# Kernel tuning notes

Measured on AMD Instinct MI355X. Metric: run time of the kernel, lower is better.

## Reference

```python
import jax, jax.numpy as jnp
import numpy as np

N_NODES = 100000
N_EDGES = 1600000
HIDDEN = 512
LOWER = 128
NUM_RELS = 6


def setup_inputs() -> dict:
    key = jax.random.key(0)
    ks = jax.random.split(key, 16)
    glorot = lambda k, shape: jax.random.normal(k, shape, jnp.float32) * (2.0 / (shape[-2] + shape[-1])) ** 0.5
    return {
        "h_origin": jax.random.normal(ks[0], (N_NODES, HIDDEN), jnp.float32),
        "edge_src": jax.random.randint(ks[1], (N_EDGES,), 0, N_NODES, jnp.int32),
        "edge_dst": jax.random.randint(ks[2], (N_EDGES,), 0, N_NODES, jnp.int32),
        "edge_type": jax.random.randint(ks[3], (N_EDGES,), 0, NUM_RELS, jnp.int32),
        "W_lower": glorot(ks[4], (HIDDEN, LOWER)),
        "b_lower": jnp.zeros((LOWER,), jnp.float32),
        "W1": glorot(ks[5], (NUM_RELS, LOWER, LOWER)),
        "b1": jnp.zeros((LOWER,), jnp.float32),
        "W2": glorot(ks[6], (NUM_RELS, LOWER, LOWER)),
        "b2": jnp.zeros((LOWER,), jnp.float32),
        "W3": glorot(ks[7], (NUM_RELS, LOWER, LOWER)),
        "b3": jnp.zeros((LOWER,), jnp.float32),
        "W_upper": glorot(ks[8], (LOWER, HIDDEN)),
        "b_upper": jnp.zeros((HIDDEN,), jnp.float32),
        "W_skip": glorot(ks[9], (HIDDEN, HIDDEN)),
        "b_skip": jnp.zeros((HIDDEN,), jnp.float32),
    }


def _ngcn_layer(h, W, b, edge_src, edge_dst, edge_type, n_nodes):
    # R-GCN layer: msg_e = h[src_e] @ W[rel_e]; h'_v = relu(sum_{e->v} msg_e + b)
    # Equivalent grouped form: transform all nodes by all relations (dense GEMMs),
    # then gather per-edge by (rel, src) -- same math as per-edge bmm.
    t = jnp.einsum("nd,rde->rne", h, W)          # [R, N, out]
    msg = t[edge_type, edge_src]                   # [E, out] gather
    agg = jax.ops.segment_sum(msg, edge_dst, num_segments=n_nodes)  # [N, out]
    return jax.nn.relu(agg + b)


def reference(h_origin, edge_src, edge_dst, edge_type,
              W_lower, b_lower, W1, b1, W2, b2, W3, b3,
              W_upper, b_upper, W_skip, b_skip):
    n_nodes = h_origin.shape[0]
    # lower: Linear + ReLU (hidden -> lower)
    h = jax.nn.relu(h_origin @ W_lower + b_lower)
    # three NGCN (R-GCN) layers, num_rels = 6
    h = _ngcn_layer(h, W1, b1, edge_src, edge_dst, edge_type, n_nodes)
    h = _ngcn_layer(h, W2, b2, edge_src, edge_dst, edge_type, n_nodes)
    h = _ngcn_layer(h, W3, b3, edge_src, edge_dst, edge_type, n_nodes)
    # upper(h) + skipper(origin): bg.ndata['h'] = upper(h) + skipper(origin_ndata)
    out = jax.nn.relu(h @ W_upper + b_upper) + jax.nn.relu(h_origin @ W_skip + b_skip)
    return out
```

## Files before the change

### kernel.cpp

```cpp
#include <hip/hip_runtime.h>
#include <hip/hip_bf16.h>

#define NN 100000
#define NE 1600000
#define HID 512
#define LOW 128
#define NR  6
#define NBINS (NN * NR)

typedef short  bf16x8 __attribute__((ext_vector_type(8)));
typedef float  f32x4  __attribute__((ext_vector_type(4)));

__device__ __forceinline__ unsigned short f2bf(float x) {
    __hip_bfloat16 h = __float2bfloat16(x);
    return __builtin_bit_cast(unsigned short, h);
}
__device__ __forceinline__ float bf2f(unsigned short u) {
    return __builtin_bit_cast(float, (unsigned int)u << 16);
}

__device__ __forceinline__ void stage_tile(const unsigned short* __restrict__ G,
                                           int r0, int k0, int Kstride, int Rmax,
                                           char* lds_base, int tid)
{
    #pragma unroll
    for (int is = 0; is < 4; ++is) {
        int L   = is * 4096 + tid * 16;
        int row = L >> 7;
        int c   = ((L >> 4) & 7) ^ (row & 7);
        int gr  = r0 + row;
        gr = (gr < Rmax) ? gr : (Rmax - 1);
        const char* src = (const char*)G + ((size_t)gr * Kstride + k0) * 2 + c * 16;
        __builtin_amdgcn_global_load_lds(
            (const __attribute__((address_space(1))) void*)src,
            (__attribute__((address_space(3))) void*)(lds_base + is * 4096 + (tid & 192) * 16),
            16, 0, 0);
    }
}

__device__ __forceinline__ bf16x8 lds_frag(const char* lds_base, int row, int clog)
{
    return *(const bf16x8*)(lds_base + row * 128 + ((clog ^ (row & 7)) << 4));
}

__global__ __launch_bounds__(256, 2)
void gemm_bf16(const unsigned short* __restrict__ A,
               const unsigned short* __restrict__ Bt,
               const float* __restrict__ bias,
               unsigned short* __restrict__ C,
               int M, int N, int K)
{
    __shared__ __align__(16) char lA[16384];
    __shared__ __align__(16) char lB[16384];

    const int tid  = threadIdx.x;
    const int lane = tid & 63;
    const int wid  = tid >> 6;
    const int wm   = wid >> 1;
    const int wn   = wid & 1;
    const int m0   = blockIdx.y * 128;
    const int n0   = blockIdx.x * 128;

    f32x4 acc[4][4] = {};

    for (int k0 = 0; k0 < K; k0 += 64) {
        stage_tile(A,  m0, k0, K, M, lA, tid);
        stage_tile(Bt, n0, k0, K, N, lB, tid);
        __syncthreads();
        #pragma unroll
        for (int kk = 0; kk < 2; ++kk) {
            const int clog = kk * 4 + (lane >> 4);
            bf16x8 af[4], bfr[4];
            #pragma unroll
            for (int i = 0; i < 4; ++i)
                af[i] = lds_frag(lA, wm * 64 + i * 16 + (lane & 15), clog);
            #pragma unroll
            for (int j = 0; j < 4; ++j)
                bfr[j] = lds_frag(lB, wn * 64 + j * 16 + (lane & 15), clog);
            #pragma unroll
            for (int i = 0; i < 4; ++i)
                #pragma unroll
                for (int j = 0; j < 4; ++j)
                    acc[i][j] = __builtin_amdgcn_mfma_f32_16x16x32_bf16(
                        af[i], bfr[j], acc[i][j], 0, 0, 0);
        }
        __syncthreads();
    }

    const int col_l = lane & 15;
    const int rgrp  = lane >> 4;
    #pragma unroll
    for (int i = 0; i < 4; ++i) {
        #pragma unroll
        for (int j = 0; j < 4; ++j) {
            int col  = n0 + wn * 64 + j * 16 + col_l;
            float bv = bias[col];
            #pragma unroll
            for (int r = 0; r < 4; ++r) {
                int row = m0 + wm * 64 + i * 16 + rgrp * 4 + r;
                if (row < M)
                    C[(size_t)row * N + col] = f2bf(fmaxf(acc[i][j][r] + bv, 0.f));
            }
        }
    }
}

__global__ __launch_bounds__(256, 2)
void gemm_out_fused(const unsigned short* __restrict__ h,
                    const unsigned short* __restrict__ Wut,
                    const float* __restrict__ bu,
                    const unsigned short* __restrict__ hob,
                    const unsigned short* __restrict__ Wst,
                    const float* __restrict__ bs,
                    float* __restrict__ out, int M)
{
    __shared__ __align__(16) char lA[16384];
    __shared__ __align__(16) char lB[16384];

    const int tid  = threadIdx.x;
    const int lane = tid & 63;
    const int wid  = tid >> 6;
    const int wm   = wid >> 1;
    const int wn   = wid & 1;
    const int m0   = blockIdx.y * 128;
    const int n0   = blockIdx.x * 128;

    f32x4 acc1[4][4] = {};
    f32x4 acc2[4][4] = {};

    for (int k0 = 0; k0 < LOW; k0 += 64) {
        stage_tile(h,   m0, k0, LOW, M,   lA, tid);
        stage_tile(Wut, n0, k0, LOW, HID, lB, tid);
        __syncthreads();
        #pragma unroll
        for (int kk = 0; kk < 2; ++kk) {
            const int clog = kk * 4 + (lane >> 4);
            bf16x8 af[4], bfr[4];
            #pragma unroll
            for (int i = 0; i < 4; ++i)
                af[i] = lds_frag(lA, wm * 64 + i * 16 + (lane & 15), clog);
            #pragma unroll
            for (int j = 0; j < 4; ++j)
                bfr[j] = lds_frag(lB, wn * 64 + j * 16 + (lane & 15), clog);
            #pragma unroll
            for (int i = 0; i < 4; ++i)
                #pragma unroll
                for (int j = 0; j < 4; ++j)
                    acc1[i][j] = __builtin_amdgcn_mfma_f32_16x16x32_bf16(
                        af[i], bfr[j], acc1[i][j], 0, 0, 0);
        }
        __syncthreads();
    }
    for (int k0 = 0; k0 < HID; k0 += 64) {
        stage_tile(hob, m0, k0, HID, M,   lA, tid);
        stage_tile(Wst, n0, k0, HID, HID, lB, tid);
        __syncthreads();
        #pragma unroll
        for (int kk = 0; kk < 2; ++kk) {
            const int clog = kk * 4 + (lane >> 4);
            bf16x8 af[4], bfr[4];
            #pragma unroll
            for (int i = 0; i < 4; ++i)
                af[i] = lds_frag(lA, wm * 64 + i * 16 + (lane & 15), clog);
            #pragma unroll
            for (int j = 0; j < 4; ++j)
                bfr[j] = lds_frag(lB, wn * 64 + j * 16 + (lane & 15), clog);
            #pragma unroll
            for (int i = 0; i < 4; ++i)
                #pragma unroll
                for (int j = 0; j < 4; ++j)
                    acc2[i][j] = __builtin_amdgcn_mfma_f32_16x16x32_bf16(
                        af[i], bfr[j], acc2[i][j], 0, 0, 0);
        }
        __syncthreads();
    }

    const int col_l = lane & 15;
    const int rgrp  = lane >> 4;
    #pragma unroll
    for (int i = 0; i < 4; ++i) {
        #pragma unroll
        for (int j = 0; j < 4; ++j) {
            int col   = n0 + wn * 64 + j * 16 + col_l;
            float bv1 = bu[col], bv2 = bs[col];
            #pragma unroll
            for (int r = 0; r < 4; ++r) {
                int row = m0 + wm * 64 + i * 16 + rgrp * 4 + r;
                if (row < M)
                    out[(size_t)row * HID + col] =
                        fmaxf(acc1[i][j][r] + bv1, 0.f) + fmaxf(acc2[i][j][r] + bv2, 0.f);
            }
        }
    }
}

__global__ __launch_bounds__(256)
void conv_f32_bf16(const float4* __restrict__ in, ushort4* __restrict__ out, int n4)
{
    for (int i = blockIdx.x * 256 + threadIdx.x; i < n4; i += gridDim.x * 256) {
        float4 v = in[i];
        ushort4 o;
        o.x = f2bf(v.x); o.y = f2bf(v.y); o.z = f2bf(v.z); o.w = f2bf(v.w);
        out[i] = o;
    }
}

__global__ __launch_bounds__(256)
void transpose_bf16(const float* __restrict__ W, unsigned short* __restrict__ Wt,
                    int R, int C)
{
    int idx = blockIdx.x * 256 + threadIdx.x;
    if (idx < R * C) {
        int r = idx / C, c = idx - r * C;
        Wt[(size_t)c * R + r] = f2bf(W[idx]);
    }
}

#define SCAN_VT 8
#define SCAN_BS 256
#define SCAN_CHUNK (SCAN_VT * SCAN_BS)
#define SCAN_NB ((NBINS + SCAN_CHUNK - 1) / SCAN_CHUNK)

__global__ __launch_bounds__(256)
void k_hist(const int* __restrict__ dst, const int* __restrict__ typ,
            int* __restrict__ deg, int E)
{
    int e = blockIdx.x * 256 + threadIdx.x;
    if (e < E) atomicAdd(&deg[dst[e] * NR + typ[e]], 1);
}

__global__ __launch_bounds__(SCAN_BS)
void k_scan_part(const int* __restrict__ deg, int* __restrict__ blocksum, int n)
{
    __shared__ int ps[SCAN_BS];
    const int t = threadIdx.x;
    const int lo = blockIdx.x * SCAN_CHUNK + t * SCAN_VT;
    int s = 0;
    #pragma unroll
    for (int k = 0; k < SCAN_VT; ++k) {
        int i = lo + k;
        if (i < n) s += deg[i];
    }
    ps[t] = s;
    __syncthreads();
    for (int off = SCAN_BS / 2; off > 0; off >>= 1) {
        if (t < off) ps[t] += ps[t + off];
        __syncthreads();
    }
    if (t == 0) blocksum[blockIdx.x] = ps[0];
}

__global__ __launch_bounds__(64)
void k_scan_mid(const int* __restrict__ blocksum, int* __restrict__ blockoff,
                int* __restrict__ rowstart, int nb, int n)
{
    if (threadIdx.x == 0) {
        int run = 0;
        for (int i = 0; i < nb; ++i) { blockoff[i] = run; run += blocksum[i]; }
        rowstart[n] = run;
    }
}

__global__ __launch_bounds__(SCAN_BS)
void k_scan_final(const int* __restrict__ deg, const int* __restrict__ blockoff,
                  int* __restrict__ rowstart, int* __restrict__ cursor, int n)
{
    __shared__ int ps[SCAN_BS];
    const int t = threadIdx.x;
    const int lo = blockIdx.x * SCAN_CHUNK + t * SCAN_VT;
    int local[SCAN_VT];
    int s = 0;
    #pragma unroll
    for (int k = 0; k < SCAN_VT; ++k) {
        int i = lo + k;
        int v = (i < n) ? deg[i] : 0;
        local[k] = v;
        s += v;
    }
    ps[t] = s;
    __syncthreads();
    for (int off = 1; off < SCAN_BS; off <<= 1) {
        int v = (t >= off) ? ps[t - off] : 0;
        __syncthreads();
        ps[t] += v;
        __syncthreads();
    }
    int run = blockoff[blockIdx.x] + ((t > 0) ? ps[t - 1] : 0);
    #pragma unroll
    for (int k = 0; k < SCAN_VT; ++k) {
        int i = lo + k;
        if (i < n) {
            rowstart[i] = run;
            cursor[i]   = run;
            run += local[k];
        }
    }
}

__global__ __launch_bounds__(256)
void k_fill(const int* __restrict__ src, const int* __restrict__ dst,
            const int* __restrict__ typ, int* __restrict__ cursor,
            int* __restrict__ list, int E)
{
    int e = blockIdx.x * 256 + threadIdx.x;
    if (e < E) {
        int pos = atomicAdd(&cursor[dst[e] * NR + typ[e]], 1);
        list[pos] = src[e];
    }
}

__global__ __launch_bounds__(256)
void gather_agg(const unsigned short* __restrict__ h,
                const int* __restrict__ rowstart,
                const int* __restrict__ list,
                unsigned short* __restrict__ S)
{
    const int v = (blockIdx.x * 256 + threadIdx.x) >> 6;
    if (v >= NN) return;
    const int lane = threadIdx.x & 63;
    const ushort2* hp = (const ushort2*)h;

    const int b0 = rowstart[v * NR + 0];
    const int b1 = rowstart[v * NR + 1];
    const int b2 = rowstart[v * NR + 2];
    const int b3 = rowstart[v * NR + 3];
    const int b4 = rowstart[v * NR + 4];
    const int b5 = rowstart[v * NR + 5];
    const int b6 = rowstart[v * NR + 6];
    const int n0 = b1 - b0, n1 = b2 - b1, n2 = b3 - b2;
    const int n3 = b4 - b3, n4 = b5 - b4, n5 = b6 - b5;
    const int kmax = max(max(max(n0, n1), max(n2, n3)), max(n4, n5));

    float ax0 = 0.f, ay0 = 0.f, ax1 = 0.f, ay1 = 0.f, ax2 = 0.f, ay2 = 0.f;
    float ax3 = 0.f, ay3 = 0.f, ax4 = 0.f, ay4 = 0.f, ax5 = 0.f, ay5 = 0.f;

    for (int k = 0; k < kmax; ++k) {
        int i0 = (k < n0) ? (b0 + k) : 0;
        int i1 = (k < n1) ? (b1 + k) : 0;
        int i2 = (k < n2) ? (b2 + k) : 0;
        int i3 = (k < n3) ? (b3 + k) : 0;
        int i4 = (k < n4) ? (b4 + k) : 0;
        int i5 = (k < n5) ? (b5 + k) : 0;
        int s0 = list[i0], s1 = list[i1], s2 = list[i2];
        int s3 = list[i3], s4 = list[i4], s5 = list[i5];
        ushort2 u0 = hp[(size_t)s0 * 64 + lane];
        ushort2 u1 = hp[(size_t)s1 * 64 + lane];
        ushort2 u2 = hp[(size_t)s2 * 64 + lane];
        ushort2 u3 = hp[(size_t)s3 * 64 + lane];
        ushort2 u4 = hp[(size_t)s4 * 64 + lane];
        ushort2 u5 = hp[(size_t)s5 * 64 + lane];
        ax0 += (k < n0) ? bf2f(u0.x) : 0.f;  ay0 += (k < n0) ? bf2f(u0.y) : 0.f;
        ax1 += (k < n1) ? bf2f(u1.x) : 0.f;  ay1 += (k < n1) ? bf2f(u1.y) : 0.f;
        ax2 += (k < n2) ? bf2f(u2.x) : 0.f;  ay2 += (k < n2) ? bf2f(u2.y) : 0.f;
        ax3 += (k < n3) ? bf2f(u3.x) : 0.f;  ay3 += (k < n3) ? bf2f(u3.y) : 0.f;
        ax4 += (k < n4) ? bf2f(u4.x) : 0.f;  ay4 += (k < n4) ? bf2f(u4.y) : 0.f;
        ax5 += (k < n5) ? bf2f(u5.x) : 0.f;  ay5 += (k < n5) ? bf2f(u5.y) : 0.f;
    }

    ushort2* o = (ushort2*)(S + (size_t)v * (NR * LOW));
    ushort2 w;
    w.x = f2bf(ax0); w.y = f2bf(ay0); o[0 * 64 + lane] = w;
    w.x = f2bf(ax1); w.y = f2bf(ay1); o[1 * 64 + lane] = w;
    w.x = f2bf(ax2); w.y = f2bf(ay2); o[2 * 64 + lane] = w;
    w.x = f2bf(ax3); w.y = f2bf(ay3); o[3 * 64 + lane] = w;
    w.x = f2bf(ax4); w.y = f2bf(ay4); o[4 * 64 + lane] = w;
    w.x = f2bf(ax5); w.y = f2bf(ay5); o[5 * 64 + lane] = w;
}

extern "C" void kernel_launch(void* const* d_in, const int* in_sizes, int n_in,
                              void* d_out, int out_size, void* d_ws, size_t ws_size,
                              hipStream_t stream)
{
    (void)in_sizes; (void)n_in; (void)out_size; (void)ws_size;

    const float* h_origin = (const float*)d_in[0];
    const int*   esrc     = (const int*)d_in[1];
    const int*   edst     = (const int*)d_in[2];
    const int*   etyp     = (const int*)d_in[3];
    const float* W_lower  = (const float*)d_in[4];
    const float* b_lower  = (const float*)d_in[5];
    const float* Wl[3]    = {(const float*)d_in[6], (const float*)d_in[8], (const float*)d_in[10]};
    const float* bl[3]    = {(const float*)d_in[7], (const float*)d_in[9], (const float*)d_in[11]};
    const float* W_upper  = (const float*)d_in[12];
    const float* b_upper  = (const float*)d_in[13];
    const float* W_skip   = (const float*)d_in[14];
    const float* b_skip   = (const float*)d_in[15];
    float*       out      = (float*)d_out;

    unsigned short* hob = (unsigned short*)d_ws;
    unsigned short* h   = hob + (size_t)NN * HID;
    unsigned short* S   = h + (size_t)NN * LOW;
    unsigned short* wlt = S + (size_t)NN * NR * LOW;
    unsigned short* w1t = wlt + (size_t)LOW * HID;
    unsigned short* w2t = w1t + (size_t)LOW * NR * LOW;
    unsigned short* w3t = w2t + (size_t)LOW * NR * LOW;
    unsigned short* wut = w3t + (size_t)LOW * NR * LOW;
    unsigned short* wst = wut + (size_t)HID * LOW;
    int* deg      = (int*)(wst + (size_t)HID * HID);
    int* rowstart = deg + NBINS;
    int* cursor   = rowstart + NBINS + 1;
    int* list     = cursor + NBINS;
    int* blocksum = list + NE;
    int* blockoff = blocksum + SCAN_NB;
    unsigned short* wtL[3] = {w1t, w2t, w3t};

    const unsigned eBlocks = (unsigned)((NE + 255) / 256);
    const unsigned mBlocks = (unsigned)((NN + 127) / 128);

    conv_f32_bf16<<<dim3(2048), dim3(256), 0, stream>>>(
        (const float4*)h_origin, (ushort4*)hob, NN * HID / 4);
    transpose_bf16<<<dim3((HID * LOW + 255) / 256), dim3(256), 0, stream>>>(
        W_lower, wlt, HID, LOW);
    for (int L = 0; L < 3; ++L)
        transpose_bf16<<<dim3((NR * LOW * LOW + 255) / 256), dim3(256), 0, stream>>>(
            Wl[L], wtL[L], NR * LOW, LOW);
    transpose_bf16<<<dim3((LOW * HID + 255) / 256), dim3(256), 0, stream>>>(
        W_upper, wut, LOW, HID);
    transpose_bf16<<<dim3((HID * HID + 255) / 256), dim3(256), 0, stream>>>(
        W_skip, wst, HID, HID);

    hipMemsetAsync(deg, 0, NBINS * sizeof(int), stream);
    k_hist<<<dim3(eBlocks), dim3(256), 0, stream>>>(edst, etyp, deg, NE);
    k_scan_part<<<dim3(SCAN_NB), dim3(SCAN_BS), 0, stream>>>(deg, blocksum, NBINS);
    k_scan_mid<<<dim3(1), dim3(64), 0, stream>>>(blocksum, blockoff, rowstart, SCAN_NB, NBINS);
    k_scan_final<<<dim3(SCAN_NB), dim3(SCAN_BS), 0, stream>>>(deg, blockoff, rowstart, cursor, NBINS);
    k_fill<<<dim3(eBlocks), dim3(256), 0, stream>>>(esrc, edst, etyp, cursor, list, NE);

    gemm_bf16<<<dim3(1, mBlocks), dim3(256), 0, stream>>>(
        hob, wlt, b_lower, h, NN, LOW, HID);

    const unsigned gBlocks = (unsigned)((NN * 64 + 255) / 256);
    for (int L = 0; L < 3; ++L) {
        gather_agg<<<dim3(gBlocks), dim3(256), 0, stream>>>(h, rowstart, list, S);
        gemm_bf16<<<dim3(1, mBlocks), dim3(256), 0, stream>>>(
            S, wtL[L], bl[L], h, NN, LOW, NR * LOW);
    }

    gemm_out_fused<<<dim3(HID / 128, mBlocks), dim3(256), 0, stream>>>(
        h, wut, b_upper, hob, wst, b_skip, out, NN);
}
```

Measured before the change: 857.4 us.

## Use 128x64 GEMM tiles with XCD swizzle and vectorize gather aggregation

The GEMMs drop from 128x128 to 128x64 output tiles, which cuts LDS and accumulator registers so occupancy can rise, and they now use a 1D grid whose block order is remapped across XCDs. The gather-aggregate kernel drops from 64 to 16 lanes per node, and each lane loads 8 bf16 values with one 16-byte access. The aim is more parallelism for the narrow N=128 GEMMs and more memory-level parallelism in the gather. In exchange, A tiles are re-read once per N tile, and the gather's per-lane register use grows. The bounds check on v was removed, which is safe only because NN*16 divides evenly into blocks of 256.

```diff
diff --git a/kernel.cpp b/kernel.cpp
--- a/kernel.cpp
+++ b/kernel.cpp
@@ -10,6 +10,8 @@
 
 typedef short  bf16x8 __attribute__((ext_vector_type(8)));
 typedef float  f32x4  __attribute__((ext_vector_type(4)));
+typedef float  f32x8  __attribute__((ext_vector_type(8)));
+typedef unsigned short u16x8 __attribute__((ext_vector_type(8)));
 
 __device__ __forceinline__ unsigned short f2bf(float x) {
     __hip_bfloat16 h = __float2bfloat16(x);
@@ -18,13 +20,20 @@
 __device__ __forceinline__ float bf2f(unsigned short u) {
     return __builtin_bit_cast(float, (unsigned int)u << 16);
 }
-
-__device__ __forceinline__ void stage_tile(const unsigned short* __restrict__ G,
+__device__ __forceinline__ f32x8 cvt8(u16x8 u) {
+    f32x8 r;
+    #pragma unroll
+    for (int i = 0; i < 8; ++i) r[i] = bf2f(u[i]);
+    return r;
+}
+
+template<int ITERS>
+__device__ __forceinline__ void stage_rows(const unsigned short* __restrict__ G,
                                            int r0, int k0, int Kstride, int Rmax,
                                            char* lds_base, int tid)
 {
     #pragma unroll
-    for (int is = 0; is < 4; ++is) {
+    for (int is = 0; is < ITERS; ++is) {
         int L   = is * 4096 + tid * 16;
         int row = L >> 7;
         int c   = ((L >> 4) & 7) ^ (row & 7);
@@ -43,44 +52,55 @@
     return *(const bf16x8*)(lds_base + row * 128 + ((clog ^ (row & 7)) << 4));
 }
 
-__global__ __launch_bounds__(256, 2)
-void gemm_bf16(const unsigned short* __restrict__ A,
-               const unsigned short* __restrict__ Bt,
-               const float* __restrict__ bias,
-               unsigned short* __restrict__ C,
-               int M, int N, int K)
+__device__ __forceinline__ int xcd_swizzle(int bid, int nwg)
+{
+    int q = nwg >> 3, r = nwg & 7;
+    int x = bid & 7;
+    int base = (x < r) ? x * (q + 1) : r * (q + 1) + (x - r) * q;
+    return base + (bid >> 3);
+}
+
+template<bool RELU>
+__global__ __launch_bounds__(256, 4)
+void gemm_bf16_64(const unsigned short* __restrict__ A,
+                  const unsigned short* __restrict__ Bt,
+                  const float* __restrict__ bias,
+                  unsigned short* __restrict__ C,
+                  int M, int N, int K, int nTiles)
 {
     __shared__ __align__(16) char lA[16384];
-    __shared__ __align__(16) char lB[16384];
+    __shared__ __align__(16) char lB[8192];
 
     const int tid  = threadIdx.x;
     const int lane = tid & 63;
     const int wid  = tid >> 6;
     const int wm   = wid >> 1;
     const int wn   = wid & 1;
-    const int m0   = blockIdx.y * 128;
-    const int n0   = blockIdx.x * 128;
-
-    f32x4 acc[4][4] = {};
+
+    const int idx = xcd_swizzle(blockIdx.x, gridDim.x);
+    const int m0  = (idx / nTiles) * 128;
+    const int n0  = (idx % nTiles) * 64;
+
+    f32x4 acc[4][2] = {};
 
     for (int k0 = 0; k0 < K; k0 += 64) {
-        stage_tile(A,  m0, k0, K, M, lA, tid);
-        stage_tile(Bt, n0, k0, K, N, lB, tid);
+        stage_rows<4>(A,  m0, k0, K, M, lA, tid);
+        stage_rows<2>(Bt, n0, k0, K, N, lB, tid);
         __syncthreads();
         #pragma unroll
         for (int kk = 0; kk < 2; ++kk) {
             const int clog = kk * 4 + (lane >> 4);
-            bf16x8 af[4], bfr[4];
+            bf16x8 af[4], bfr[2];
             #pragma unroll
             for (int i = 0; i < 4; ++i)
                 af[i] = lds_frag(lA, wm * 64 + i * 16 + (lane & 15), clog);
             #pragma unroll
-            for (int j = 0; j < 4; ++j)
-                bfr[j] = lds_frag(lB, wn * 64 + j * 16 + (lane & 15), clog);
+            for (int j = 0; j < 2; ++j)
+                bfr[j] = lds_frag(lB, wn * 32 + j * 16 + (lane & 15), clog);
             #pragma unroll
             for (int i = 0; i < 4; ++i)
                 #pragma unroll
-                for (int j = 0; j < 4; ++j)
+                for (int j = 0; j < 2; ++j)
                     acc[i][j] = __builtin_amdgcn_mfma_f32_16x16x32_bf16(
                         af[i], bfr[j], acc[i][j], 0, 0, 0);
         }
@@ -92,20 +112,23 @@
     #pragma unroll
     for (int i = 0; i < 4; ++i) {
         #pragma unroll
-        for (int j = 0; j < 4; ++j) {
-            int col  = n0 + wn * 64 + j * 16 + col_l;
-            float bv = bias[col];
+        for (int j = 0; j < 2; ++j) {
+            int col  = n0 + wn * 32 + j * 16 + col_l;
+            float bv = RELU ? bias[col] : 0.f;
             #pragma unroll
             for (int r = 0; r < 4; ++r) {
                 int row = m0 + wm * 64 + i * 16 + rgrp * 4 + r;
-                if (row < M)
-                    C[(size_t)row * N + col] = f2bf(fmaxf(acc[i][j][r] + bv, 0.f));
+                if (row < M) {
+                    float v = acc[i][j][r];
+                    if constexpr (RELU) v = fmaxf(v + bv, 0.f);
+                    C[(size_t)row * N + col] = f2bf(v);
+                }
             }
         }
     }
 }
 
-__global__ __launch_bounds__(256, 2)
+__global__ __launch_bounds__(256, 3)
 void gemm_out_fused(const unsigned short* __restrict__ h,
                     const unsigned short* __restrict__ Wut,
                     const float* __restrict__ bu,
@@ -115,60 +138,62 @@
                     float* __restrict__ out, int M)
 {
     __shared__ __align__(16) char lA[16384];
-    __shared__ __align__(16) char lB[16384];
+    __shared__ __align__(16) char lB[8192];
 
     const int tid  = threadIdx.x;
     const int lane = tid & 63;
     const int wid  = tid >> 6;
     const int wm   = wid >> 1;
     const int wn   = wid & 1;
-    const int m0   = blockIdx.y * 128;
-    const int n0   = blockIdx.x * 128;
-
-    f32x4 acc1[4][4] = {};
-    f32x4 acc2[4][4] = {};
+
+    const int idx = xcd_swizzle(blockIdx.x, gridDim.x);
+    const int m0  = (idx >> 3) * 128;
+    const int n0  = (idx & 7) * 64;
+
+    f32x4 acc1[4][2] = {};
+    f32x4 acc2[4][2] = {};
 
     for (int k0 = 0; k0 < LOW; k0 += 64) {
-        stage_tile(h,   m0, k0, LOW, M,   lA, tid);
-        stage_tile(Wut, n0, k0, LOW, HID, lB, tid);
+        stage_rows<4>(h,   m0, k0, LOW, M,   lA, tid);
+        stage_rows<2>(Wut, n0, k0, LOW, HID, lB, tid);
         __syncthreads();
         #pragma unroll
         for (int kk = 0; kk < 2; ++kk) {
             const int clog = kk * 4 + (lane >> 4);
-            bf16x8 af[4], bfr[4];
+            bf16x8 af[4], bfr[2];
             #pragma unroll
             for (int i = 0; i < 4; ++i)
                 af[i] = lds_frag(lA, wm * 64 + i * 16 + (lane & 15), clog);
             #pragma unroll
-            for (int j = 0; j < 4; ++j)
-                bfr[j] = lds_frag(lB, wn * 64 + j * 16 + (lane & 15), clog);
+            for (int j = 0; j < 2; ++j)
+                bfr[j] = lds_frag(lB, wn * 32 + j * 16 + (lane & 15), clog);
             #pragma unroll
             for (int i = 0; i < 4; ++i)
                 #pragma unroll
-                for (int j = 0; j < 4; ++j)
+                for (int j = 0; j < 2; ++j)
                     acc1[i][j] = __builtin_amdgcn_mfma_f32_16x16x32_bf16(
                         af[i], bfr[j], acc1[i][j], 0, 0, 0);
         }
         __syncthreads();
     }
     for (int k0 = 0; k0 < HID; k0 += 64) {
-        stage_tile(hob, m0, k0, HID, M,   lA, tid);
-        stage_tile(Wst, n0, k0, HID, HID, lB, tid);
+        stage_rows<4>(hob, m0, k0, HID, M,   lA, tid);
+        stage_rows<2>(Wst, n0, k0, HID, HID, lB, tid);
         __syncthreads();
         #pragma unroll
         for (int kk = 0; kk < 2; ++kk) {
             const int clog = kk * 4 + (lane >> 4);
-            bf16x8 af[4], bfr[4];
+            bf16x8 af[4], bfr[2];
             #pragma unroll
             for (int i = 0; i < 4; ++i)
                 af[i] = lds_frag(lA, wm * 64 + i * 16 + (lane & 15), clog);
             #pragma unroll
-            for (int j = 0; j < 4; ++j)
-                bfr[j] = lds_frag(lB, wn * 64 + j * 16 + (lane & 15), clog);
+            for (int j = 0; j < 2; ++j)
+                bfr[j] = lds_frag(lB, wn * 32 + j * 16 + (lane & 15), clog);
             #pragma unroll
             for (int i = 0; i < 4; ++i)
                 #pragma unroll
-                for (int j = 0; j < 4; ++j)
+                for (int j = 0; j < 2; ++j)
                     acc2[i][j] = __builtin_amdgcn_mfma_f32_16x16x32_bf16(
                         af[i], bfr[j], acc2[i][j], 0, 0, 0);
         }
@@ -180,8 +205,8 @@
     #pragma unroll
     for (int i = 0; i < 4; ++i) {
         #pragma unroll
-        for (int j = 0; j < 4; ++j) {
-            int col   = n0 + wn * 64 + j * 16 + col_l;
+        for (int j = 0; j < 2; ++j) {
+            int col   = n0 + wn * 32 + j * 16 + col_l;
             float bv1 = bu[col], bv2 = bs[col];
             #pragma unroll
             for (int r = 0; r < 4; ++r) {
@@ -315,10 +340,9 @@
                 const int* __restrict__ list,
                 unsigned short* __restrict__ S)
 {
-    const int v = (blockIdx.x * 256 + threadIdx.x) >> 6;
-    if (v >= NN) return;
-    const int lane = threadIdx.x & 63;
-    const ushort2* hp = (const ushort2*)h;
+    const int v = (blockIdx.x * 256 + threadIdx.x) >> 4;
+    const int lane = threadIdx.x & 15;
+    const u16x8* hp = (const u16x8*)h;
 
     const int b0 = rowstart[v * NR + 0];
     const int b1 = rowstart[v * NR + 1];
@@ -331,8 +355,7 @@
     const int n3 = b4 - b3, n4 = b5 - b4, n5 = b6 - b5;
     const int kmax = max(max(max(n0, n1), max(n2, n3)), max(n4, n5));
 
-    float ax0 = 0.f, ay0 = 0.f, ax1 = 0.f, ay1 = 0.f, ax2 = 0.f, ay2 = 0.f;
-    float ax3 = 0.f, ay3 = 0.f, ax4 = 0.f, ay4 = 0.f, ax5 = 0.f, ay5 = 0.f;
+    f32x8 a0 = {}, a1 = {}, a2 = {}, a3 = {}, a4 = {}, a5 = {};
 
     for (int k = 0; k < kmax; ++k) {
         int i0 = (k < n0) ? (b0 + k) : 0;
@@ -343,28 +366,40 @@
         int i5 = (k < n5) ? (b5 + k) : 0;
         int s0 = list[i0], s1 = list[i1], s2 = list[i2];
         int s3 = list[i3], s4 = list[i4], s5 = list[i5];
-        ushort2 u0 = hp[(size_t)s0 * 64 + lane];
-        ushort2 u1 = hp[(size_t)s1 * 64 + lane];
-        ushort2 u2 = hp[(size_t)s2 * 64 + lane];
-        ushort2 u3 = hp[(size_t)s3 * 64 + lane];
-        ushort2 u4 = hp[(size_t)s4 * 64 + lane];
-        ushort2 u5 = hp[(size_t)s5 * 64 + lane];
-        ax0 += (k < n0) ? bf2f(u0.x) : 0.f;  ay0 += (k < n0) ? bf2f(u0.y) : 0.f;
-        ax1 += (k < n1) ? bf2f(u1.x) : 0.f;  ay1 += (k < n1) ? bf2f(u1.y) : 0.f;
-        ax2 += (k < n2) ? bf2f(u2.x) : 0.f;  ay2 += (k < n2) ? bf2f(u2.y) : 0.f;
-        ax3 += (k < n3) ? bf2f(u3.x) : 0.f;  ay3 += (k < n3) ? bf2f(u3.y) : 0.f;
-        ax4 += (k < n4) ? bf2f(u4.x) : 0.f;  ay4 += (k < n4) ? bf2f(u4.y) : 0.f;
-        ax5 += (k < n5) ? bf2f(u5.x) : 0.f;  ay5 += (k < n5) ? bf2f(u5.y) : 0.f;
-    }
-
-    ushort2* o = (ushort2*)(S + (size_t)v * (NR * LOW));
-    ushort2 w;
-    w.x = f2bf(ax0); w.y = f2bf(ay0); o[0 * 64 + lane] = w;
-    w.x = f2bf(ax1); w.y = f2bf(ay1); o[1 * 64 + lane] = w;
-    w.x = f2bf(ax2); w.y = f2bf(ay2); o[2 * 64 + lane] = w;
-    w.x = f2bf(ax3); w.y = f2bf(ay3); o[3 * 64 + lane] = w;
-    w.x = f2bf(ax4); w.y = f2bf(ay4); o[4 * 64 + lane] = w;
-    w.x = f2bf(ax5); w.y = f2bf(ay5); o[5 * 64 + lane] = w;
+        u16x8 u0 = hp[(size_t)s0 * 16 + lane];
+        u16x8 u1 = hp[(size_t)s1 * 16 + lane];
+        u16x8 u2 = hp[(size_t)s2 * 16 + lane];
+        u16x8 u3 = hp[(size_t)s3 * 16 + lane];
+        u16x8 u4 = hp[(size_t)s4 * 16 + lane];
+        u16x8 u5 = hp[(size_t)s5 * 16 + lane];
+        if (k < n0) a0 += cvt8(u0);
+        if (k < n1) a1 += cvt8(u1);
+        if (k < n2) a2 += cvt8(u2);
+        if (k < n3) a3 += cvt8(u3);
+        if (k < n4) a4 += cvt8(u4);
+        if (k < n5) a5 += cvt8(u5);
+    }
+
+    u16x8* o = (u16x8*)(S + (size_t)v * (NR * LOW));
+    u16x8 w;
+    #pragma unroll
+    for (int i = 0; i < 8; ++i) w[i] = f2bf(a0[i]);
+    o[0 * 16 + lane] = w;
+    #pragma unroll
+    for (int i = 0; i < 8; ++i) w[i] = f2bf(a1[i]);
+    o[1 * 16 + lane] = w;
+    #pragma unroll
+    for (int i = 0; i < 8; ++i) w[i] = f2bf(a2[i]);
+    o[2 * 16 + lane] = w;
+    #pragma unroll
+    for (int i = 0; i < 8; ++i) w[i] = f2bf(a3[i]);
+    o[3 * 16 + lane] = w;
+    #pragma unroll
+    for (int i = 0; i < 8; ++i) w[i] = f2bf(a4[i]);
+    o[4 * 16 + lane] = w;
+    #pragma unroll
+    for (int i = 0; i < 8; ++i) w[i] = f2bf(a5[i]);
+    o[5 * 16 + lane] = w;
 }
 
 extern "C" void kernel_launch(void* const* d_in, const int* in_sizes, int n_in,
@@ -426,16 +461,16 @@
     k_scan_final<<<dim3(SCAN_NB), dim3(SCAN_BS), 0, stream>>>(deg, blockoff, rowstart, cursor, NBINS);
     k_fill<<<dim3(eBlocks), dim3(256), 0, stream>>>(esrc, edst, etyp, cursor, list, NE);
 
-    gemm_bf16<<<dim3(1, mBlocks), dim3(256), 0, stream>>>(
-        hob, wlt, b_lower, h, NN, LOW, HID);
-
-    const unsigned gBlocks = (unsigned)((NN * 64 + 255) / 256);
+    gemm_bf16_64<true><<<dim3(mBlocks * 2), dim3(256), 0, stream>>>(
+        hob, wlt, b_lower, h, NN, LOW, HID, 2);
+
+    const unsigned gBlocks = (unsigned)(((size_t)NN * 16 + 255) / 256);
     for (int L = 0; L < 3; ++L) {
         gather_agg<<<dim3(gBlocks), dim3(256), 0, stream>>>(h, rowstart, list, S);
-        gemm_bf16<<<dim3(1, mBlocks), dim3(256), 0, stream>>>(
-            S, wtL[L], bl[L], h, NN, LOW, NR * LOW);
-    }
-
-    gemm_out_fused<<<dim3(HID / 128, mBlocks), dim3(256), 0, stream>>>(
+        gemm_bf16_64<true><<<dim3(mBlocks * 2), dim3(256), 0, stream>>>(
+            S, wtL[L], bl[L], h, NN, LOW, NR * LOW, 2);
+    }
+
+    gemm_out_fused<<<dim3(mBlocks * 8), dim3(256), 0, stream>>>(
         h, wut, b_upper, hob, wst, b_skip, out, NN);
 }
```

Result: no change. 866.6 us (+1.1%).
